# Kernel optimization log

Measured on AMD Instinct MI355X. Metric: run time of the kernel, lower is better.

The kernel has to match this reference:

```python
import jax, jax.numpy as jnp
import numpy as np

B, L, D = 1, 4096, 2048
H, KV, HD = 16, 4, 128
WINDOW = 1024
ROPE_BASE = 10000.0


def _rms_norm(x, scale):
    var = jnp.mean(jnp.square(x), axis=-1, keepdims=True)
    return x * jax.lax.rsqrt(var + 1e-6) * scale


def _apply_rope(x, positions, base_frequency):
    # x: (B, L, N, HD); positions: (B, L)
    head_dim = x.shape[-1]
    half = head_dim // 2
    freq_exp = 2.0 * jnp.arange(half, dtype=jnp.float32) / head_dim
    timescale = base_frequency ** freq_exp                       # (half,)
    sinusoid = positions[..., None].astype(jnp.float32) / timescale  # (B, L, half)
    sin = jnp.sin(sinusoid)[:, :, None, :]                       # (B, L, 1, half)
    cos = jnp.cos(sinusoid)[:, :, None, :]
    x1, x2 = x[..., :half], x[..., half:]
    return jnp.concatenate([x1 * cos - x2 * sin, x2 * cos + x1 * sin], axis=-1)


def setup_inputs() -> dict:
    key = jax.random.key(0)
    ks = jax.random.split(key, 5)
    x = jax.random.normal(ks[0], (B, L, D), dtype=jnp.float32)
    positions = jnp.broadcast_to(jnp.arange(L, dtype=jnp.int32), (B, L))
    s = D ** -0.5
    Wq = jax.random.normal(ks[1], (D, H * HD), dtype=jnp.float32) * s
    Wk = jax.random.normal(ks[2], (D, KV * HD), dtype=jnp.float32) * s
    Wv = jax.random.normal(ks[3], (D, KV * HD), dtype=jnp.float32) * s
    Wo = jax.random.normal(ks[4], (H * HD, D), dtype=jnp.float32) * ((H * HD) ** -0.5)
    q_scale = jnp.ones((HD,), dtype=jnp.float32)
    k_scale = jnp.ones((HD,), dtype=jnp.float32)
    return {"x": x, "positions": positions, "Wq": Wq, "Wk": Wk, "Wv": Wv,
            "Wo": Wo, "q_scale": q_scale, "k_scale": k_scale}


def reference(x, positions, Wq, Wk, Wv, Wo, q_scale, k_scale):
    q = (x @ Wq).reshape(B, L, H, HD)
    k = (x @ Wk).reshape(B, L, KV, HD)
    v = (x @ Wv).reshape(B, L, KV, HD)

    q = _apply_rope(_rms_norm(q, q_scale), positions, ROPE_BASE)
    k = _apply_rope(_rms_norm(k, k_scale), positions, ROPE_BASE)

    rep = H // KV
    k = jnp.repeat(k, rep, axis=2)   # (B, L, H, HD)
    v = jnp.repeat(v, rep, axis=2)

    scale = HD ** -0.5
    scores = jnp.einsum('bqhd,bkhd->bhqk', q, k) * scale  # (B, H, L, L)

    idx = jnp.arange(L)
    causal = idx[:, None] >= idx[None, :]
    window = idx[None, :] >= idx[:, None] - (WINDOW - 1)
    mask = causal & window
    scores = jnp.where(mask[None, None, :, :], scores, jnp.finfo(scores.dtype).min)
    attn = jax.nn.softmax(scores, axis=-1)

    out = jnp.einsum('bhqk,bkhd->bqhd', attn, v).reshape(B, L, H * HD)
    return out @ Wo
```

## Files before the change

kernel.cpp:

```cpp
#include <hip/hip_runtime.h>
#include <cstdint>
#include <cstddef>

typedef unsigned short u16;
typedef __attribute__((ext_vector_type(4))) float  float4v;
typedef __attribute__((ext_vector_type(4))) int    int4v;
typedef __attribute__((ext_vector_type(8))) short  short8v;
typedef __attribute__((ext_vector_type(4))) short  short4v;

#define L_SEQ 4096
#define NH 16
#define NKV 4
#define WND 1024

static __device__ __forceinline__ u16 f2bf(float f) {
  union { float f; unsigned u; } v; v.f = f;
  unsigned r = (v.u + 0x7FFFu + ((v.u >> 16) & 1u)) >> 16;
  return (u16)r;
}
static __device__ __forceinline__ u16 f2bf_fast(float f) {
  union { float f; unsigned u; } v; v.f = f;
  return (u16)((v.u + 0x8000u) >> 16);
}
static __device__ __forceinline__ float bf2f(u16 b) {
  union { unsigned u; float f; } v; v.u = ((unsigned)b) << 16;
  return v.f;
}

__global__ __launch_bounds__(256) void k_prep(const float* __restrict__ x,
    u16* __restrict__ xb,
    const float* __restrict__ Wq, const float* __restrict__ Wk,
    const float* __restrict__ Wv, const float* __restrict__ Wo,
    u16* __restrict__ Wt, u16* __restrict__ Wot) {
  __shared__ float tile[64][65];
  int b = blockIdx.x;
  if (b < 8192) {
    int i = b * 256 + threadIdx.x;
    float4v v = ((const float4v*)x)[i];
    short4v o;
    o[0] = (short)f2bf(v[0]); o[1] = (short)f2bf(v[1]);
    o[2] = (short)f2bf(v[2]); o[3] = (short)f2bf(v[3]);
    ((short4v*)xb)[i] = o;
    return;
  }
  b -= 8192;
  const float* in; u16* out; int N, row_off, bx, by;
  const int K = 2048;
  if (b < 1024)      { in = Wq; out = Wt;  N = 2048; row_off = 0;    bx = b & 31; by = b >> 5; }
  else if (b < 1280) { b -= 1024; in = Wk; out = Wt;  N = 512; row_off = 2048; bx = b & 7; by = b >> 3; }
  else if (b < 1536) { b -= 1280; in = Wv; out = Wt;  N = 512; row_off = 2560; bx = b & 7; by = b >> 3; }
  else               { b -= 1536; in = Wo; out = Wot; N = 2048; row_off = 0;   bx = b & 31; by = b >> 5; }
  int n0 = bx * 64, k0 = by * 64;
  int tx = threadIdx.x & 63, ty = threadIdx.x >> 6;
#pragma unroll
  for (int i = 0; i < 16; i++)
    tile[ty + i*4][tx] = in[(size_t)(k0 + ty + i*4)*N + n0 + tx];
  __syncthreads();
#pragma unroll
  for (int i = 0; i < 16; i++)
    out[(size_t)(row_off + n0 + ty + i*4)*K + k0 + tx] = f2bf(tile[tx][ty + i*4]);
}

template<int BF16_OUT>
__global__ __launch_bounds__(256) void k_gemm_bt(const u16* __restrict__ A,
                                                 const u16* __restrict__ B,
                                                 void* __restrict__ Cv,
                                                 int M, int N, int K) {
  __shared__ alignas(16) u16 As[128*64];
  __shared__ alignas(16) u16 Bs[128*64];
  int tid = threadIdx.x;
  int lane = tid & 63, wave = tid >> 6;
  int lr = lane & 15, lg = lane >> 4;
  int m0 = blockIdx.y * 128, n0 = blockIdx.x * 128;
  int wm = (wave >> 1) * 64, wn = (wave & 1) * 64;

  float4v acc[4][4];
#pragma unroll
  for (int i = 0; i < 4; i++)
#pragma unroll
    for (int j = 0; j < 4; j++)
#pragma unroll
      for (int r = 0; r < 4; r++) acc[i][j][r] = 0.f;

  for (int kt = 0; kt < K; kt += 64) {
    __syncthreads();
#pragma unroll
    for (int it = 0; it < 4; it++) {
      int s = it*256 + tid;
      int row = s >> 3, j = s & 7;
      int col = ((j ^ (row & 7)) << 3);
      __builtin_amdgcn_global_load_lds(
          (const __attribute__((address_space(1))) void*)(A + (size_t)(m0 + row)*K + kt + col),
          (__attribute__((address_space(3))) void*)(&As[s * 8]), 16, 0, 0);
      __builtin_amdgcn_global_load_lds(
          (const __attribute__((address_space(1))) void*)(B + (size_t)(n0 + row)*K + kt + col),
          (__attribute__((address_space(3))) void*)(&Bs[s * 8]), 16, 0, 0);
    }
    __syncthreads();
#pragma unroll
    for (int half = 0; half < 2; half++) {
      short8v af[4], bf[4];
#pragma unroll
      for (int i = 0; i < 4; i++) {
        int row = wm + i*16 + lr;
        af[i] = *(const short8v*)(&As[row*64 + ((((half<<2)|lg) ^ (row & 7)) << 3)]);
      }
#pragma unroll
      for (int j = 0; j < 4; j++) {
        int row = wn + j*16 + lr;
        bf[j] = *(const short8v*)(&Bs[row*64 + ((((half<<2)|lg) ^ (row & 7)) << 3)]);
      }
#pragma unroll
      for (int i = 0; i < 4; i++)
#pragma unroll
        for (int j = 0; j < 4; j++)
          acc[i][j] = __builtin_amdgcn_mfma_f32_16x16x32_bf16(af[i], bf[j], acc[i][j], 0, 0, 0);
    }
  }
#pragma unroll
  for (int i = 0; i < 4; i++)
#pragma unroll
    for (int j = 0; j < 4; j++)
#pragma unroll
      for (int r = 0; r < 4; r++) {
        size_t idx = (size_t)(m0 + wm + i*16 + lg*4 + r)*N + (n0 + wn + j*16 + lr);
        if (BF16_OUT) ((u16*)Cv)[idx] = f2bf(acc[i][j][r]);
        else          ((float*)Cv)[idx] = acc[i][j][r];
      }
}

__global__ __launch_bounds__(256) void k_post(const u16* __restrict__ qkvb,
    const int* __restrict__ positions, const float* __restrict__ q_scale,
    const float* __restrict__ k_scale, u16* __restrict__ qb,
    u16* __restrict__ kb, u16* __restrict__ vT) {
  __shared__ u16 tile[64][66];
  int b = blockIdx.x;
  if (b >= 1024) {
    int i = b - 1024;
    int p0 = (i & 63) * 64, d0 = (i >> 6) * 64;
    int tx = threadIdx.x & 63, ty = threadIdx.x >> 6;
#pragma unroll
    for (int k = 0; k < 16; k++)
      tile[ty + k*4][tx] = qkvb[(size_t)(p0 + ty + k*4)*3072 + 2560 + d0 + tx];
    __syncthreads();
#pragma unroll
    for (int k = 0; k < 16; k++)
      vT[(size_t)(d0 + ty + k*4)*L_SEQ + p0 + tx] = tile[tx][ty + k*4];
    return;
  }
  int p = b * 4 + (threadIdx.x >> 6);
  int l = threadIdx.x & 63;
  const float LOG2_BASE = 13.287712379549449f;
  float ang = (float)positions[p] * exp2f(-(float)l * (LOG2_BASE / 64.0f));
  float sn, cs; sincosf(ang, &sn, &cs);
  float qs1 = q_scale[l], qs2 = q_scale[l + 64];
  float ks1 = k_scale[l], ks2 = k_scale[l + 64];
  const u16* base = qkvb + (size_t)p * 3072;
  const float qsc = 0.12751741505539613f;
#pragma unroll
  for (int h = 0; h < 16; h++) {
    float x1 = bf2f(base[h*128 + l]), x2 = bf2f(base[h*128 + l + 64]);
    float ss = x1*x1 + x2*x2;
#pragma unroll
    for (int m = 1; m < 64; m <<= 1) ss += __shfl_xor(ss, m);
    float rinv = rsqrtf(ss * (1.0f/128.0f) + 1e-6f);
    x1 *= rinv * qs1; x2 *= rinv * qs2;
    u16* dst = qb + ((size_t)p*NH + h)*128;
    dst[l]      = f2bf((x1*cs - x2*sn) * qsc);
    dst[l + 64] = f2bf((x2*cs + x1*sn) * qsc);
  }
#pragma unroll
  for (int g = 0; g < 4; g++) {
    float x1 = bf2f(base[2048 + g*128 + l]), x2 = bf2f(base[2048 + g*128 + l + 64]);
    float ss = x1*x1 + x2*x2;
#pragma unroll
    for (int m = 1; m < 64; m <<= 1) ss += __shfl_xor(ss, m);
    float rinv = rsqrtf(ss * (1.0f/128.0f) + 1e-6f);
    x1 *= rinv * ks1; x2 *= rinv * ks2;
    u16* dst = kb + ((size_t)p*NKV + g)*128;
    dst[l]      = f2bf(x1*cs - x2*sn);
    dst[l + 64] = f2bf(x2*cs + x1*sn);
  }
}

__global__ __launch_bounds__(256) void k_attn(const u16* __restrict__ qb,
    const u16* __restrict__ kb, const u16* __restrict__ vT,
    u16* __restrict__ ob) {
  __shared__ alignas(16) u16 Ks[64*128];
  __shared__ alignas(16) u16 Vs[128*64];
  __shared__ alignas(16) u16 Pw[4][2][16*72];
  int tid = threadIdx.x;
  int lane = tid & 63, wave = tid >> 6;
  int lr = lane & 15, lg = lane >> 4;
  int flat = blockIdx.x;
  int xcd = flat & 7, slot = flat >> 3;
  int gh = xcd >> 1;
  int q0 = ((xcd & 1) * 64 + slot) * 32;
  int h = gh * 4 + wave;

  short8v qf[2][4];
#pragma unroll
  for (int m = 0; m < 2; m++) {
    const u16* qrow = qb + ((size_t)(q0 + m*16 + lr)*NH + h)*128 + lg*8;
#pragma unroll
    for (int t = 0; t < 4; t++) qf[m][t] = *(const short8v*)(qrow + t*32);
  }

  const short one_bf = (short)0x3F80;
  const short8v ones = {one_bf,one_bf,one_bf,one_bf,one_bf,one_bf,one_bf,one_bf};

  float4v O[9][2];
#pragma unroll
  for (int dt = 0; dt < 9; dt++)
#pragma unroll
    for (int m = 0; m < 2; m++)
#pragma unroll
      for (int r = 0; r < 4; r++) O[dt][m][r] = 0.f;

  int kstart = q0 - (WND - 1); if (kstart < 0) kstart = 0; kstart &= ~63;
  for (int kt = kstart; kt < q0 + 32; kt += 64) {
    __syncthreads();
#pragma unroll
    for (int it = 0; it < 4; it++) {
      int s = it*256 + tid;
      { int row = s >> 4, j = s & 15, col = (j ^ (row & 15)) << 3;
        __builtin_amdgcn_global_load_lds(
            (const __attribute__((address_space(1))) void*)(kb + (size_t)(kt + row)*512 + gh*128 + col),
            (__attribute__((address_space(3))) void*)(&Ks[s * 8]), 16, 0, 0); }
      { int row = s >> 3, j = s & 7, col = (j ^ (row & 7)) << 3;
        __builtin_amdgcn_global_load_lds(
            (const __attribute__((address_space(1))) void*)(vT + (size_t)(gh*128 + row)*L_SEQ + kt + col),
            (__attribute__((address_space(3))) void*)(&Vs[s * 8]), 16, 0, 0); }
    }
    __syncthreads();

    float4v S[2][4];
#pragma unroll
    for (int m = 0; m < 2; m++)
#pragma unroll
      for (int t2 = 0; t2 < 4; t2++)
#pragma unroll
        for (int r = 0; r < 4; r++) S[m][t2][r] = 0.f;
#pragma unroll
    for (int t2 = 0; t2 < 4; t2++) {
      int row = t2*16 + lr;
#pragma unroll
      for (int t = 0; t < 4; t++) {
        short8v kf = *(const short8v*)(&Ks[row*128 + (((t*4 + lg) ^ (row & 15)) << 3)]);
        S[0][t2] = __builtin_amdgcn_mfma_f32_16x16x32_bf16(qf[0][t], kf, S[0][t2], 0, 0, 0);
        S[1][t2] = __builtin_amdgcn_mfma_f32_16x16x32_bf16(qf[1][t], kf, S[1][t2], 0, 0, 0);
      }
    }

    bool need_mask = (kt + 64 > q0) || (kt < q0 - (WND - 32));
    if (need_mask) {
#pragma unroll
      for (int m = 0; m < 2; m++)
#pragma unroll
        for (int r = 0; r < 4; r++) {
          int pos = q0 + m*16 + lg*4 + r;
#pragma unroll
          for (int t2 = 0; t2 < 4; t2++) {
            int key = kt + t2*16 + lr;
            float p = (key > pos || key < pos - (WND - 1)) ? 0.f : exp2f(S[m][t2][r]);
            Pw[wave][m][(lg*4 + r)*72 + t2*16 + lr] = f2bf_fast(p);
          }
        }
    } else {
#pragma unroll
      for (int m = 0; m < 2; m++)
#pragma unroll
        for (int r = 0; r < 4; r++)
#pragma unroll
          for (int t2 = 0; t2 < 4; t2++)
            Pw[wave][m][(lg*4 + r)*72 + t2*16 + lr] = f2bf_fast(exp2f(S[m][t2][r]));
    }

    short8v pf[2][2];
#pragma unroll
    for (int m = 0; m < 2; m++)
#pragma unroll
      for (int sub = 0; sub < 2; sub++)
        pf[m][sub] = *(const short8v*)(&Pw[wave][m][lr*72 + sub*32 + lg*8]);

#pragma unroll
    for (int sub = 0; sub < 2; sub++)
#pragma unroll
      for (int dt = 0; dt < 8; dt++) {
        int row = dt*16 + lr;
        short8v vf = *(const short8v*)(&Vs[row*64 + (((sub*4 + lg) ^ (row & 7)) << 3)]);
        O[dt][0] = __builtin_amdgcn_mfma_f32_16x16x32_bf16(pf[0][sub], vf, O[dt][0], 0, 0, 0);
        O[dt][1] = __builtin_amdgcn_mfma_f32_16x16x32_bf16(pf[1][sub], vf, O[dt][1], 0, 0, 0);
      }
#pragma unroll
    for (int m = 0; m < 2; m++) {
      O[8][m] = __builtin_amdgcn_mfma_f32_16x16x32_bf16(pf[m][0], ones, O[8][m], 0, 0, 0);
      O[8][m] = __builtin_amdgcn_mfma_f32_16x16x32_bf16(pf[m][1], ones, O[8][m], 0, 0, 0);
    }
  }

#pragma unroll
  for (int m = 0; m < 2; m++)
#pragma unroll
    for (int r = 0; r < 4; r++) {
      float inv = 1.0f / O[8][m][r];
#pragma unroll
      for (int dt = 0; dt < 8; dt++)
        ob[((size_t)(q0 + m*16 + lg*4 + r)*NH + h)*128 + dt*16 + lr] =
            f2bf(O[dt][m][r] * inv);
    }
}

extern "C" void kernel_launch(void* const* d_in, const int* in_sizes, int n_in,
                              void* d_out, int out_size, void* d_ws, size_t ws_size,
                              hipStream_t stream) {
  (void)in_sizes; (void)n_in; (void)out_size; (void)ws_size;
  const float* x        = (const float*)d_in[0];
  const int*   positions= (const int*)d_in[1];
  const float* Wq       = (const float*)d_in[2];
  const float* Wk       = (const float*)d_in[3];
  const float* Wv       = (const float*)d_in[4];
  const float* Wo       = (const float*)d_in[5];
  const float* q_scale  = (const float*)d_in[6];
  const float* k_scale  = (const float*)d_in[7];
  float* out = (float*)d_out;

  char* ws = (char*)d_ws;
  u16* xb   = (u16*)ws; ws += (size_t)4096*2048*2;
  u16* Wt   = (u16*)ws; ws += (size_t)3072*2048*2;
  u16* Wot  = (u16*)ws; ws += (size_t)2048*2048*2;
  u16* qkvb = (u16*)ws; ws += (size_t)4096*3072*2;
  u16* qb   = (u16*)ws; ws += (size_t)4096*2048*2;
  u16* kb   = (u16*)ws; ws += (size_t)4096*512*2;
  u16* vT   = (u16*)ws; ws += (size_t)4096*512*2;
  u16* ob   = qkvb;

  k_prep<<<10752, 256, 0, stream>>>(x, xb, Wq, Wk, Wv, Wo, Wt, Wot);
  k_gemm_bt<1><<<dim3(24,32), 256, 0, stream>>>(xb, Wt, qkvb, 4096, 3072, 2048);
  k_post<<<1536, 256, 0, stream>>>(qkvb, positions, q_scale, k_scale, qb, kb, vT);
  k_attn<<<512, 256, 0, stream>>>(qb, kb, vT, ob);
  k_gemm_bt<0><<<dim3(16,32), 256, 0, stream>>>(ob, Wot, out, 4096, 2048, 2048);
}
```

Baseline: 302.0 us.

## Prefetch next K/V tile into registers while computing current attention tile

Replaces the synchronous global_load_lds tile fill with a register-staged software pipeline. The next K/V tile is loaded into registers before the QK^T and PV MFMAs run, then written to LDS after compute. It also raises wave priority around the MFMA blocks with s_setprio. The aim is to hide global load latency behind compute, at the cost of more VGPRs, possibly lower occupancy, and two barriers per iteration.

```diff
diff --git a/kernel.cpp b/kernel.cpp
--- a/kernel.cpp
+++ b/kernel.cpp
@@ -218,21 +218,37 @@
       for (int r = 0; r < 4; r++) O[dt][m][r] = 0.f;
 
   int kstart = q0 - (WND - 1); if (kstart < 0) kstart = 0; kstart &= ~63;
-  for (int kt = kstart; kt < q0 + 32; kt += 64) {
-    __syncthreads();
-#pragma unroll
-    for (int it = 0; it < 4; it++) {
-      int s = it*256 + tid;
-      { int row = s >> 4, j = s & 15, col = (j ^ (row & 15)) << 3;
-        __builtin_amdgcn_global_load_lds(
-            (const __attribute__((address_space(1))) void*)(kb + (size_t)(kt + row)*512 + gh*128 + col),
-            (__attribute__((address_space(3))) void*)(&Ks[s * 8]), 16, 0, 0); }
-      { int row = s >> 3, j = s & 7, col = (j ^ (row & 7)) << 3;
-        __builtin_amdgcn_global_load_lds(
-            (const __attribute__((address_space(1))) void*)(vT + (size_t)(gh*128 + row)*L_SEQ + kt + col),
-            (__attribute__((address_space(3))) void*)(&Vs[s * 8]), 16, 0, 0); }
-    }
-    __syncthreads();
+  int kend = q0 + 32;
+
+  short8v kreg[4], vreg[4];
+
+#define TILE_LOAD(KT)                                                          \
+  _Pragma("unroll")                                                            \
+  for (int it = 0; it < 4; it++) {                                             \
+    int s = it*256 + tid;                                                      \
+    int krow = s >> 4, kj = s & 15;                                            \
+    kreg[it] = *(const short8v*)(kb + (size_t)((KT) + krow)*512 + gh*128 +     \
+                                 ((kj ^ (krow & 15)) << 3));                   \
+    int vrow = s >> 3, vj = s & 7;                                             \
+    vreg[it] = *(const short8v*)(vT + (size_t)(gh*128 + vrow)*L_SEQ + (KT) +   \
+                                 ((vj ^ (vrow & 7)) << 3));                    \
+  }
+
+#define TILE_STORE()                                                           \
+  _Pragma("unroll")                                                            \
+  for (int it = 0; it < 4; it++) {                                             \
+    int s = it*256 + tid;                                                      \
+    *(short8v*)(&Ks[s*8]) = kreg[it];                                          \
+    *(short8v*)(&Vs[s*8]) = vreg[it];                                          \
+  }
+
+  TILE_LOAD(kstart);
+  TILE_STORE();
+  __syncthreads();
+
+  for (int kt = kstart; kt < kend; kt += 64) {
+    bool has_next = (kt + 64 < kend);
+    if (has_next) { TILE_LOAD(kt + 64); }
 
     float4v S[2][4];
 #pragma unroll
@@ -241,6 +257,7 @@
       for (int t2 = 0; t2 < 4; t2++)
 #pragma unroll
         for (int r = 0; r < 4; r++) S[m][t2][r] = 0.f;
+    __builtin_amdgcn_s_setprio(1);
 #pragma unroll
     for (int t2 = 0; t2 < 4; t2++) {
       int row = t2*16 + lr;
@@ -251,6 +268,7 @@
         S[1][t2] = __builtin_amdgcn_mfma_f32_16x16x32_bf16(qf[1][t], kf, S[1][t2], 0, 0, 0);
       }
     }
+    __builtin_amdgcn_s_setprio(0);
 
     bool need_mask = (kt + 64 > q0) || (kt < q0 - (WND - 32));
     if (need_mask) {
@@ -283,6 +301,7 @@
       for (int sub = 0; sub < 2; sub++)
         pf[m][sub] = *(const short8v*)(&Pw[wave][m][lr*72 + sub*32 + lg*8]);
 
+    __builtin_amdgcn_s_setprio(1);
 #pragma unroll
     for (int sub = 0; sub < 2; sub++)
 #pragma unroll
@@ -297,6 +316,13 @@
       O[8][m] = __builtin_amdgcn_mfma_f32_16x16x32_bf16(pf[m][0], ones, O[8][m], 0, 0, 0);
       O[8][m] = __builtin_amdgcn_mfma_f32_16x16x32_bf16(pf[m][1], ones, O[8][m], 0, 0, 0);
     }
+    __builtin_amdgcn_s_setprio(0);
+
+    if (has_next) {
+      __syncthreads();
+      TILE_STORE();
+      __syncthreads();
+    }
   }
 
 #pragma unroll
@@ -309,6 +335,8 @@
         ob[((size_t)(q0 + m*16 + lg*4 + r)*NH + h)*128 + dt*16 + lr] =
             f2bf(O[dt][m][r] * inv);
     }
+#undef TILE_LOAD
+#undef TILE_STORE
 }
 
 extern "C" void kernel_launch(void* const* d_in, const int* in_sizes, int n_in,
```

After: 326.9 us. 8.3% more time.

## Double-buffer K tiles and prefetch next K/V during attention compute

Applied to the files above, without the earlier changes.

Adds a second LDS buffer for K and issues the next tile's K loads before the QK^T MFMAs. The next V tile is loaded right after the PV MFMAs, using explicit vmcnt waits and barriers in place of the two syncthreads per iteration. The aim is to hide global-to-LDS load latency behind matrix work. The cost is extra LDS per block, which may lower occupancy, and fragile hand-tuned waitcnt accounting, though the counts look consistent.

```diff
diff --git a/kernel.cpp b/kernel.cpp
--- a/kernel.cpp
+++ b/kernel.cpp
@@ -186,7 +186,7 @@
 __global__ __launch_bounds__(256) void k_attn(const u16* __restrict__ qb,
     const u16* __restrict__ kb, const u16* __restrict__ vT,
     u16* __restrict__ ob) {
-  __shared__ alignas(16) u16 Ks[64*128];
+  __shared__ alignas(16) u16 Ks[2][64*128];
   __shared__ alignas(16) u16 Vs[128*64];
   __shared__ alignas(16) u16 Pw[4][2][16*72];
   int tid = threadIdx.x;
@@ -218,21 +218,38 @@
       for (int r = 0; r < 4; r++) O[dt][m][r] = 0.f;
 
   int kstart = q0 - (WND - 1); if (kstart < 0) kstart = 0; kstart &= ~63;
-  for (int kt = kstart; kt < q0 + 32; kt += 64) {
-    __syncthreads();
-#pragma unroll
-    for (int it = 0; it < 4; it++) {
-      int s = it*256 + tid;
-      { int row = s >> 4, j = s & 15, col = (j ^ (row & 15)) << 3;
-        __builtin_amdgcn_global_load_lds(
-            (const __attribute__((address_space(1))) void*)(kb + (size_t)(kt + row)*512 + gh*128 + col),
-            (__attribute__((address_space(3))) void*)(&Ks[s * 8]), 16, 0, 0); }
-      { int row = s >> 3, j = s & 7, col = (j ^ (row & 7)) << 3;
-        __builtin_amdgcn_global_load_lds(
-            (const __attribute__((address_space(1))) void*)(vT + (size_t)(gh*128 + row)*L_SEQ + kt + col),
-            (__attribute__((address_space(3))) void*)(&Vs[s * 8]), 16, 0, 0); }
-    }
-    __syncthreads();
+  int kend = q0 + 32;
+
+#define STAGE_K(KT, BUF)                                                       \
+  _Pragma("unroll")                                                            \
+  for (int it = 0; it < 4; it++) {                                             \
+    int s = it*256 + tid;                                                      \
+    int row = s >> 4, j = s & 15, col = (j ^ (row & 15)) << 3;                 \
+    __builtin_amdgcn_global_load_lds(                                          \
+        (const __attribute__((address_space(1))) void*)(kb + (size_t)((KT) + row)*512 + gh*128 + col), \
+        (__attribute__((address_space(3))) void*)(&Ks[BUF][s * 8]), 16, 0, 0); \
+  }
+#define STAGE_V(KT)                                                            \
+  _Pragma("unroll")                                                            \
+  for (int it = 0; it < 4; it++) {                                             \
+    int s = it*256 + tid;                                                      \
+    int row = s >> 3, j = s & 7, col = (j ^ (row & 7)) << 3;                   \
+    __builtin_amdgcn_global_load_lds(                                          \
+        (const __attribute__((address_space(1))) void*)(vT + (size_t)(gh*128 + row)*L_SEQ + (KT) + col), \
+        (__attribute__((address_space(3))) void*)(&Vs[s * 8]), 16, 0, 0);      \
+  }
+
+  STAGE_K(kstart, 0);
+  STAGE_V(kstart);
+
+  int par = 0;
+  for (int kt = kstart; kt < kend; kt += 64, par ^= 1) {
+    bool has_next = (kt + 64 < kend);
+
+    asm volatile("s_waitcnt vmcnt(4)" ::: "memory");
+    __builtin_amdgcn_sched_barrier(0);
+    __builtin_amdgcn_s_barrier();
+    if (has_next) { STAGE_K(kt + 64, par ^ 1); }
 
     float4v S[2][4];
 #pragma unroll
@@ -246,7 +263,7 @@
       int row = t2*16 + lr;
 #pragma unroll
       for (int t = 0; t < 4; t++) {
-        short8v kf = *(const short8v*)(&Ks[row*128 + (((t*4 + lg) ^ (row & 15)) << 3)]);
+        short8v kf = *(const short8v*)(&Ks[par][row*128 + (((t*4 + lg) ^ (row & 15)) << 3)]);
         S[0][t2] = __builtin_amdgcn_mfma_f32_16x16x32_bf16(qf[0][t], kf, S[0][t2], 0, 0, 0);
         S[1][t2] = __builtin_amdgcn_mfma_f32_16x16x32_bf16(qf[1][t], kf, S[1][t2], 0, 0, 0);
       }
@@ -283,6 +300,11 @@
       for (int sub = 0; sub < 2; sub++)
         pf[m][sub] = *(const short8v*)(&Pw[wave][m][lr*72 + sub*32 + lg*8]);
 
+    if (has_next) asm volatile("s_waitcnt vmcnt(4)" ::: "memory");
+    else          asm volatile("s_waitcnt vmcnt(0)" ::: "memory");
+    __builtin_amdgcn_sched_barrier(0);
+    __builtin_amdgcn_s_barrier();
+
 #pragma unroll
     for (int sub = 0; sub < 2; sub++)
 #pragma unroll
@@ -297,6 +319,9 @@
       O[8][m] = __builtin_amdgcn_mfma_f32_16x16x32_bf16(pf[m][0], ones, O[8][m], 0, 0, 0);
       O[8][m] = __builtin_amdgcn_mfma_f32_16x16x32_bf16(pf[m][1], ones, O[8][m], 0, 0, 0);
     }
+
+    __builtin_amdgcn_s_barrier();
+    if (has_next) { STAGE_V(kt + 64); }
   }
 
 #pragma unroll
@@ -309,6 +334,8 @@
         ob[((size_t)(q0 + m*16 + lg*4 + r)*NH + h)*128 + dt*16 + lr] =
             f2bf(O[dt][m][r] * inv);
     }
+#undef STAGE_K
+#undef STAGE_V
 }
 
 extern "C" void kernel_launch(void* const* d_in, const int* in_sizes, int n_in,
```

Measured after the change: 333.0 us. +10.3%, slower.
